# Performance work log

Measured on AMD Instinct MI355X. Metric: run time of the kernel, lower is better.

## Reference

```python
import jax, jax.numpy as jnp
import numpy as np

N_NODES = 100000
N_EDGES = 1600000
F_IN, H1, H2, N_CLS = 512, 180, 120, 40
NEG_SLOPE = 0.01  # F.leaky_relu default


def setup_inputs() -> dict:
    key = jax.random.key(0)
    ks = jax.random.split(key, 8)
    x = jax.random.normal(ks[0], (N_NODES, F_IN), dtype=jnp.float32)
    edge_index = jax.random.randint(ks[1], (2, N_EDGES), 0, N_NODES, dtype=jnp.int64)
    W1 = jax.random.normal(ks[2], (F_IN, H1), dtype=jnp.float32) / np.sqrt(F_IN)
    b1 = jnp.zeros((H1,), dtype=jnp.float32)
    W2 = jax.random.normal(ks[3], (H1, H2), dtype=jnp.float32) / np.sqrt(H1)
    b2 = jnp.zeros((H2,), dtype=jnp.float32)
    W3 = jax.random.normal(ks[4], (H2, N_CLS), dtype=jnp.float32) / np.sqrt(H2)
    b3 = jnp.zeros((N_CLS,), dtype=jnp.float32)
    return {"x": x, "edge_index": edge_index, "W1": W1, "b1": b1,
            "W2": W2, "b2": b2, "W3": W3, "b3": b3}


def _add_self_loops(edge_index, n):
    loop = jnp.arange(n, dtype=edge_index.dtype)
    src = jnp.concatenate([edge_index[0], loop])
    dst = jnp.concatenate([edge_index[1], loop])
    return src, dst


def _gcn_conv(h, src, dst, norm, W, b, n):
    # PyG GCNConv: linear transform first, then normalized scatter-add at dst.
    h = h @ W  # [N, out]
    msg = norm[:, None] * h[src]  # gather at source, per-edge scale
    out = jax.ops.segment_sum(msg, dst, num_segments=n)  # scatter-add at dest
    return out + b


def reference(x, edge_index, W1, b1, W2, b2, W3, b3):
    n = x.shape[0]
    src, dst = _add_self_loops(edge_index, n)
    # symmetric normalization deg^-1/2 * deg^-1/2 on self-loop-augmented graph
    ones = jnp.ones(dst.shape[0], dtype=x.dtype)
    deg = jax.ops.segment_sum(ones, dst, num_segments=n)
    dinv = jnp.where(deg > 0, jax.lax.rsqrt(deg), 0.0)
    norm = dinv[src] * dinv[dst]  # [E+N]

    h = _gcn_conv(x, src, dst, norm, W1, b1, n)
    h = jnp.where(h >= 0, h, NEG_SLOPE * h)
    h = _gcn_conv(h, src, dst, norm, W2, b2, n)
    h = jnp.where(h >= 0, h, NEG_SLOPE * h)
    logits = h @ W3 + b3
    return jax.nn.log_softmax(logits, axis=1)
```

## Files before the change

kernel.cpp:

```cpp
#include <hip/hip_runtime.h>
#include <math.h>

typedef __attribute__((ext_vector_type(8))) short short8;
typedef __attribute__((ext_vector_type(4))) float f32x4;

static constexpr int F_IN = 512;
static constexpr int H1V = 180, H1P = 192;
static constexpr int H2V = 120, H2P = 128;
static constexpr int NC  = 40,  NCP = 64;

__device__ inline unsigned f2bf(float f) {
    unsigned u = __float_as_uint(f);
    return (u + 0x7fffu + ((u >> 16) & 1u)) >> 16;
}
__device__ inline unsigned cvtpk(float lo, float hi) {
    unsigned r;
    asm("v_cvt_pk_bf16_f32 %0, %1, %2" : "=v"(r) : "v"(lo), "v"(hi));
    return r;
}
#define BLO(u) __uint_as_float((u) << 16)
#define BHI(u) __uint_as_float((u) & 0xffff0000u)

__device__ inline void gload_lds16(const void* gsrc, void* ldst) {
    __builtin_amdgcn_global_load_lds(
        (const __attribute__((address_space(1))) void*)gsrc,
        (__attribute__((address_space(3))) void*)ldst, 16, 0, 0);
}

__global__ void k_init(const int* __restrict__ ei, int* __restrict__ flag,
                       const float* __restrict__ W1, const float* __restrict__ W2,
                       const float* __restrict__ W3, const float* __restrict__ b1,
                       const float* __restrict__ b2, const float* __restrict__ b3,
                       unsigned short* __restrict__ W1s, unsigned short* __restrict__ W2s,
                       unsigned short* __restrict__ W3s, float* __restrict__ b1p,
                       float* __restrict__ b2p, float* __restrict__ b3p) {
    if (blockIdx.x < 16) {
        int i = blockIdx.x * 256 + threadIdx.x;
        if (ei[2 * i + 1] != 0) flag[0] = 1;
        return;
    }
    const int n1 = F_IN * H1P;
    const int n2 = n1 + H1P * H2P;
    const int n3 = n2 + H2P * NCP;
    const int n4 = n3 + H1P;
    const int n5 = n4 + H2P;
    const int n6 = n5 + NCP;
    int i = (blockIdx.x - 16) * 256 + threadIdx.x;
    if (i < n1) {
        int k = i / H1P, c = i % H1P;
        float v = (c < H1V) ? W1[k * H1V + c] : 0.0f;
        W1s[(size_t)(k >> 3) * H1P * 8 + c * 8 + (k & 7)] = (unsigned short)f2bf(v);
    } else if (i < n2) {
        int j = i - n1;
        int k = j / H2P, c = j % H2P;
        float v = (k < H1V && c < H2V) ? W2[k * H2V + c] : 0.0f;
        W2s[(size_t)(k >> 3) * H2P * 8 + c * 8 + (k & 7)] = (unsigned short)f2bf(v);
    } else if (i < n3) {
        int j = i - n2;
        int k = j / NCP, c = j % NCP;
        float v = (k < H2V && c < NC) ? W3[k * NC + c] : 0.0f;
        W3s[(size_t)(k >> 3) * NCP * 8 + c * 8 + (k & 7)] = (unsigned short)f2bf(v);
    } else if (i < n4) {
        int c = i - n3;
        b1p[c] = (c < H1V) ? b1[c] : 0.0f;
    } else if (i < n5) {
        int c = i - n4;
        b2p[c] = (c < H2V) ? b2[c] : 0.0f;
    } else if (i < n6) {
        int c = i - n5;
        b3p[c] = (c < NC) ? b3[c] : -1e30f;
    }
}

__global__ __launch_bounds__(256) void k_megaA(const float* __restrict__ X,
                                               const short8* __restrict__ Bs,
                                               signed char* __restrict__ Hq,
                                               float* __restrict__ sc, int M, int gb,
                                               const int* __restrict__ ei, int E,
                                               const int* __restrict__ flag,
                                               int* __restrict__ deg,
                                               int* __restrict__ dst32,
                                               uint2* __restrict__ sr,
                                               int interleave) {
    __shared__ float ldsf[6144];
    int bid;
    bool isGemm;
    if (interleave) {
        int g = blockIdx.x / 3, r = blockIdx.x % 3;
        if (r == 0) { isGemm = true; bid = g; }
        else        { isGemm = false; bid = g * 2 + r - 1; }
    } else {
        isGemm = (int)blockIdx.x < gb;
        bid = isGemm ? blockIdx.x : blockIdx.x - gb;
    }

    if (!isGemm) {
        int e = bid * 256 + threadIdx.x;
        if (e >= E) return;
        bool i64 = (flag[0] == 0);
        int s, d;
        if (i64) { s = ei[2 * e]; d = ei[2 * E + 2 * e]; }
        else     { s = ei[e];     d = ei[E + e]; }
        int r = atomicAdd(&deg[d], 1);
        dst32[e] = d;
        sr[e] = make_uint2((unsigned)s, (unsigned)r);
        return;
    }

    char* lds = (char*)ldsf;
    int t = threadIdx.x;
    int w = t >> 6, l = t & 63;
    int lr = l & 15, kg = l >> 4;
    int row0 = bid * 32;
    int colb = w * 48;

    f32x4 acc[2][3];
#pragma unroll
    for (int m = 0; m < 2; ++m)
#pragma unroll
        for (int nn = 0; nn < 3; ++nn) acc[m][nn] = (f32x4){0.f, 0.f, 0.f, 0.f};

    auto stage = [&](int kb, int buf) {
#pragma unroll
        for (int j = 0; j < 2; ++j) {
            int o = j * 4096 + t * 16;
            int row = o >> 8;
            int col4 = ((o >> 4) & 15) ^ (row & 15);
            int rowg = row0 + row;
            if (rowg >= M) rowg = M - 1;
            gload_lds16(X + (size_t)rowg * F_IN + kb + col4 * 4,
                        lds + buf * 8192 + j * 4096 + w * 1024);
        }
    };

    short8 breg[2][2][3];
    auto loadB = [&](int ts, int pp) {
#pragma unroll
        for (int kk = 0; kk < 2; ++kk)
#pragma unroll
            for (int nn = 0; nn < 3; ++nn)
                breg[pp][kk][nn] =
                    Bs[(size_t)(ts * 8 + kk * 4 + kg) * H1P + colb + nn * 16 + lr];
    };

    auto compute = [&](int cur, int pp) {
#pragma unroll
        for (int kk = 0; kk < 2; ++kk) {
            short8 a[2];
#pragma unroll
            for (int m = 0; m < 2; ++m) {
                int row = m * 16 + lr;
                char* base = lds + cur * 8192 + row * 256;
                int c0 = kk * 8 + kg * 2;
                float4 v0 = *(const float4*)(base + (((c0 + 0) ^ (row & 15)) * 16));
                float4 v1 = *(const float4*)(base + (((c0 + 1) ^ (row & 15)) * 16));
                union { unsigned u[4]; short8 s; } cu;
                cu.u[0] = cvtpk(v0.x, v0.y);
                cu.u[1] = cvtpk(v0.z, v0.w);
                cu.u[2] = cvtpk(v1.x, v1.y);
                cu.u[3] = cvtpk(v1.z, v1.w);
                a[m] = cu.s;
            }
#pragma unroll
            for (int m = 0; m < 2; ++m)
#pragma unroll
                for (int nn = 0; nn < 3; ++nn)
                    acc[m][nn] = __builtin_amdgcn_mfma_f32_16x16x32_bf16(
                        a[m], breg[pp][kk][nn], acc[m][nn], 0, 0, 0);
        }
    };

    stage(0, 0);
    stage(64, 1);
    loadB(0, 0);
    asm volatile("s_waitcnt vmcnt(8)" ::: "memory");
    __builtin_amdgcn_s_barrier();
    __builtin_amdgcn_sched_barrier(0);

#pragma unroll
    for (int ts = 0; ts < 8; ++ts) {
        if (ts < 6) stage((ts + 2) * 64, (ts + 2) % 3);
        if (ts < 7) loadB(ts + 1, (ts + 1) & 1);
        compute(ts % 3, ts & 1);
        if (ts < 7) {
            if (ts < 6) {
                asm volatile("s_waitcnt vmcnt(8)" ::: "memory");
            } else {
                asm volatile("s_waitcnt vmcnt(6)" ::: "memory");
            }
            __builtin_amdgcn_s_barrier();
            __builtin_amdgcn_sched_barrier(0);
        }
    }

    __syncthreads();
    float* rmaxp = (float*)lds;
#pragma unroll
    for (int m = 0; m < 2; ++m) {
#pragma unroll
        for (int j = 0; j < 4; ++j) {
            int rl = m * 16 + kg * 4 + j;
            float lm = 0.f;
#pragma unroll
            for (int nn = 0; nn < 3; ++nn)
                lm = fmaxf(lm, fabsf(acc[m][nn][j]));
#pragma unroll
            for (int d = 1; d < 16; d <<= 1)
                lm = fmaxf(lm, __shfl_xor(lm, d));
            if (lr == 0) rmaxp[rl * 4 + w] = lm;
        }
    }
    __syncthreads();
#pragma unroll
    for (int m = 0; m < 2; ++m) {
#pragma unroll
        for (int j = 0; j < 4; ++j) {
            int rl = m * 16 + kg * 4 + j;
            int grow = row0 + rl;
            if (grow >= M) continue;
            float rm = fmaxf(fmaxf(rmaxp[rl * 4 + 0], rmaxp[rl * 4 + 1]),
                             fmaxf(rmaxp[rl * 4 + 2], rmaxp[rl * 4 + 3]));
            float inv = (rm > 0.f) ? 127.0f / rm : 0.f;
            if (w == 0 && lr == 0) sc[grow] = rm * (1.0f / 127.0f);
#pragma unroll
            for (int nn = 0; nn < 3; ++nn) {
                float v = acc[m][nn][j] * inv;
                v = fminf(fmaxf(rintf(v), -127.f), 127.f);
                Hq[(size_t)grow * H1P + colb + nn * 16 + lr] = (signed char)(int)v;
            }
        }
    }
}

__global__ void k_scan1(const int* __restrict__ deg, int* __restrict__ rp,
                        int* __restrict__ bsum, float* __restrict__ dinv,
                        const float* __restrict__ sc, float* __restrict__ scd,
                        int n) {
    __shared__ int s[256];
    int t = threadIdx.x;
    int base = blockIdx.x * 1024 + t * 4;
    int v0 = (base + 0 < n) ? deg[base + 0] : 0;
    int v1 = (base + 1 < n) ? deg[base + 1] : 0;
    int v2 = (base + 2 < n) ? deg[base + 2] : 0;
    int v3 = (base + 3 < n) ? deg[base + 3] : 0;
    if (base + 0 < n) { float d = rsqrtf((float)(v0 + 1)); dinv[base + 0] = d; scd[base + 0] = d * sc[base + 0]; }
    if (base + 1 < n) { float d = rsqrtf((float)(v1 + 1)); dinv[base + 1] = d; scd[base + 1] = d * sc[base + 1]; }
    if (base + 2 < n) { float d = rsqrtf((float)(v2 + 1)); dinv[base + 2] = d; scd[base + 2] = d * sc[base + 2]; }
    if (base + 3 < n) { float d = rsqrtf((float)(v3 + 1)); dinv[base + 3] = d; scd[base + 3] = d * sc[base + 3]; }
    int sum = v0 + v1 + v2 + v3;
    s[t] = sum;
    __syncthreads();
    for (int off = 1; off < 256; off <<= 1) {
        int x = (t >= off) ? s[t - off] : 0;
        __syncthreads();
        s[t] += x;
        __syncthreads();
    }
    int run = s[t] - sum;
    if (t == 255) bsum[blockIdx.x] = s[255];
    if (base + 0 < n) rp[base + 0] = run; run += v0;
    if (base + 1 < n) rp[base + 1] = run; run += v1;
    if (base + 2 < n) rp[base + 2] = run; run += v2;
    if (base + 3 < n) rp[base + 3] = run;
}

__global__ void k_scan3(const int* __restrict__ bsum, int* __restrict__ rp,
                        int n, int E, int nb) {
    __shared__ int s[128], ov[128];
    int t = threadIdx.x;
    if (t < 128) {
        int v = (t < nb) ? bsum[t] : 0;
        s[t] = v; ov[t] = v;
    }
    __syncthreads();
    for (int off = 1; off < 128; off <<= 1) {
        int x = 0;
        if (t < 128 && t >= off) x = s[t - off];
        __syncthreads();
        if (t < 128) s[t] += x;
        __syncthreads();
    }
    int i = blockIdx.x * 256 + t;
    if (i < n) {
        int b = i >> 10;
        rp[i] += s[b] - ov[b];
    } else if (i == n) {
        rp[n] = E;
    }
}

__global__ __launch_bounds__(256) void k_fill(const int* __restrict__ dst32,
                                              const uint2* __restrict__ sr, int E,
                                              const int* __restrict__ rp,
                                              int* __restrict__ csr,
                                              int bw, int chunk) {
    int bkt = blockIdx.x & 7;
    int lo = bkt * bw, hi = lo + bw;
    int ch = blockIdx.x >> 3;
    int e0 = ch * chunk;
    int e1 = min(E, e0 + chunk);
    for (int e = e0 + (int)threadIdx.x; e < e1; e += 256) {
        int d = dst32[e];
        if (d >= lo && d < hi) {
            uint2 v = sr[e];
            csr[rp[d] + (int)v.y] = (int)v.x;
        }
    }
}

__global__ __launch_bounds__(256) void k_gat1q(const signed char* __restrict__ Hq,
                                               const float* __restrict__ scd,
                                               const float* __restrict__ dinv,
                                               const int* __restrict__ rp,
                                               const int* __restrict__ csr,
                                               const float* __restrict__ bias,
                                               uint2* __restrict__ out, int n) {
    int wv = threadIdx.x >> 6, l = threadIdx.x & 63;
    int i = blockIdx.x * 4 + wv;
    if (i >= n) return;
    bool act = l < 48;
    int c = act ? l : 0;
    const unsigned* Hr = (const unsigned*)(Hq + c * 4);

    float a0, a1, a2, a3;
    {
        unsigned w0 = Hr[(size_t)i * 48];
        float s0 = scd[i];
        a0 = (float)(signed char)(w0) * s0;
        a1 = (float)(signed char)(w0 >> 8) * s0;
        a2 = (float)(signed char)(w0 >> 16) * s0;
        a3 = (float)(signed char)(w0 >> 24) * s0;
    }
    float p0 = 0.f, p1 = 0.f, p2 = 0.f, p3 = 0.f;

    int e0 = rp[i], e1 = rp[i + 1];
    int e = e0;
    for (; e + 7 < e1; e += 8) {
        int s[8];
#pragma unroll
        for (int q = 0; q < 8; ++q) s[q] = csr[e + q];
        float scs[8];
#pragma unroll
        for (int q = 0; q < 8; ++q) scs[q] = scd[s[q]];
        unsigned v[8];
#pragma unroll
        for (int q = 0; q < 8; ++q) v[q] = Hr[(size_t)s[q] * 48];
#pragma unroll
        for (int q = 0; q < 8; q += 2) {
            a0 = fmaf((float)(signed char)(v[q]), scs[q], a0);
            a1 = fmaf((float)(signed char)(v[q] >> 8), scs[q], a1);
            a2 = fmaf((float)(signed char)(v[q] >> 16), scs[q], a2);
            a3 = fmaf((float)(signed char)(v[q] >> 24), scs[q], a3);
            p0 = fmaf((float)(signed char)(v[q + 1]), scs[q + 1], p0);
            p1 = fmaf((float)(signed char)(v[q + 1] >> 8), scs[q + 1], p1);
            p2 = fmaf((float)(signed char)(v[q + 1] >> 16), scs[q + 1], p2);
            p3 = fmaf((float)(signed char)(v[q + 1] >> 24), scs[q + 1], p3);
        }
    }
    for (; e < e1; ++e) {
        int s0 = csr[e];
        float sq = scd[s0];
        unsigned w0 = Hr[(size_t)s0 * 48];
        a0 = fmaf((float)(signed char)(w0), sq, a0);
        a1 = fmaf((float)(signed char)(w0 >> 8), sq, a1);
        a2 = fmaf((float)(signed char)(w0 >> 16), sq, a2);
        a3 = fmaf((float)(signed char)(w0 >> 24), sq, a3);
    }
    a0 += p0; a1 += p1; a2 += p2; a3 += p3;

    float di = dinv[i];
    float4 bb = *(const float4*)(bias + 4 * c);
    float o0 = fmaf(di, a0, bb.x);
    float o1 = fmaf(di, a1, bb.y);
    float o2 = fmaf(di, a2, bb.z);
    float o3 = fmaf(di, a3, bb.w);
    o0 = o0 >= 0.f ? o0 : 0.01f * o0;
    o1 = o1 >= 0.f ? o1 : 0.01f * o1;
    o2 = o2 >= 0.f ? o2 : 0.01f * o2;
    o3 = o3 >= 0.f ? o3 : 0.01f * o3;
    if (act) {
        uint2 r;
        r.x = (f2bf(o1) << 16) | f2bf(o0);
        r.y = (f2bf(o3) << 16) | f2bf(o2);
        out[(size_t)i * 48 + c] = r;
    }
}

__global__ __launch_bounds__(512) void k_gemm2(const unsigned short* __restrict__ A,
                                               const short8* __restrict__ Bs,
                                               const float* __restrict__ dinv,
                                               unsigned short* __restrict__ Hout,
                                               int M) {
    __shared__ unsigned short ldsu[16384];
    char* lds = (char*)ldsu;
    int t = threadIdx.x;
    int w = t >> 6, l = t & 63;
    int lr = l & 15, kg = l >> 4;
    int wr = w >> 2, wc = w & 3;
    int row0 = blockIdx.x * 128;
    int colb = wc * 32;

    f32x4 acc[4][2];
#pragma unroll
    for (int m = 0; m < 4; ++m)
#pragma unroll
        for (int nn = 0; nn < 2; ++nn) acc[m][nn] = (f32x4){0.f, 0.f, 0.f, 0.f};

    auto stage = [&](int kb, int buf) {
#pragma unroll
        for (int j = 0; j < 2; ++j) {
            int o = j * 8192 + t * 16;
            int row = o >> 7;
            int chunk = ((o >> 4) & 7) ^ (row & 7);
            int rowg = row0 + row;
            if (rowg >= M) rowg = M - 1;
            gload_lds16(A + (size_t)rowg * H1P + kb + chunk * 8,
                        lds + buf * 16384 + j * 8192 + w * 1024);
        }
    };

    stage(0, 0);
    __syncthreads();

    for (int ts = 0; ts < 3; ++ts) {
        int cur = ts & 1;
        if (ts < 2) stage((ts + 1) * 64, cur ^ 1);
        short8 b[2][2];
#pragma unroll
        for (int kk = 0; kk < 2; ++kk)
#pragma unroll
            for (int nn = 0; nn < 2; ++nn)
                b[kk][nn] = Bs[(size_t)(ts * 8 + kk * 4 + kg) * H2P + colb + nn * 16 + lr];
        short8 a[2][4];
#pragma unroll
        for (int kk = 0; kk < 2; ++kk)
#pragma unroll
            for (int m = 0; m < 4; ++m) {
                int row = wr * 64 + m * 16 + lr;
                a[kk][m] = *(const short8*)(lds + cur * 16384 + row * 128 +
                                            (((kk * 4 + kg) ^ (row & 7)) * 16));
            }
#pragma unroll
        for (int kk = 0; kk < 2; ++kk)
#pragma unroll
            for (int m = 0; m < 4; ++m)
#pragma unroll
                for (int nn = 0; nn < 2; ++nn)
                    acc[m][nn] = __builtin_amdgcn_mfma_f32_16x16x32_bf16(a[kk][m], b[kk][nn], acc[m][nn], 0, 0, 0);
        __syncthreads();
    }

#pragma unroll
    for (int m = 0; m < 4; ++m) {
        int r4 = row0 + wr * 64 + m * 16 + kg * 4;
#pragma unroll
        for (int j = 0; j < 4; ++j) {
            int grow = r4 + j;
            if (grow < M) {
                float dv = dinv[grow];
#pragma unroll
                for (int nn = 0; nn < 2; ++nn)
                    Hout[(size_t)grow * H2P + colb + nn * 16 + lr] =
                        (unsigned short)f2bf(acc[m][nn][j] * dv);
            }
        }
    }
}

__global__ __launch_bounds__(256) void k_gat2(const uint2* __restrict__ H,
                                              const float* __restrict__ dinv,
                                              const int* __restrict__ rp,
                                              const int* __restrict__ csr,
                                              const float* __restrict__ bias,
                                              uint2* __restrict__ out, int n) {
    int wv = threadIdx.x >> 6, l = threadIdx.x & 63;
    int half = l >> 5, c = l & 31;
    int i = blockIdx.x * 8 + wv * 2 + half;
    if (i >= n) return;
    const uint2* Hr = H + c;

    float a0, a1, a2, a3;
    {
        uint2 v = Hr[(size_t)i * 32];
        a0 = BLO(v.x); a1 = BHI(v.x); a2 = BLO(v.y); a3 = BHI(v.y);
    }
    float p0 = 0.f, p1 = 0.f, p2 = 0.f, p3 = 0.f;

    int e0 = rp[i], e1 = rp[i + 1];
    int e = e0;
    for (; e + 7 < e1; e += 8) {
        int s[8];
#pragma unroll
        for (int q = 0; q < 8; ++q) s[q] = csr[e + q];
        uint2 v[8];
#pragma unroll
        for (int q = 0; q < 8; ++q) v[q] = Hr[(size_t)s[q] * 32];
#pragma unroll
        for (int q = 0; q < 8; q += 2) {
            a0 += BLO(v[q].x); a1 += BHI(v[q].x); a2 += BLO(v[q].y); a3 += BHI(v[q].y);
            p0 += BLO(v[q + 1].x); p1 += BHI(v[q + 1].x); p2 += BLO(v[q + 1].y); p3 += BHI(v[q + 1].y);
        }
    }
    for (; e + 3 < e1; e += 4) {
        int s0 = csr[e], s1 = csr[e + 1], s2 = csr[e + 2], s3 = csr[e + 3];
        uint2 va = Hr[(size_t)s0 * 32];
        uint2 vb = Hr[(size_t)s1 * 32];
        uint2 vc = Hr[(size_t)s2 * 32];
        uint2 vd = Hr[(size_t)s3 * 32];
        a0 += BLO(va.x); a1 += BHI(va.x); a2 += BLO(va.y); a3 += BHI(va.y);
        p0 += BLO(vb.x); p1 += BHI(vb.x); p2 += BLO(vb.y); p3 += BHI(vb.y);
        a0 += BLO(vc.x); a1 += BHI(vc.x); a2 += BLO(vc.y); a3 += BHI(vc.y);
        p0 += BLO(vd.x); p1 += BHI(vd.x); p2 += BLO(vd.y); p3 += BHI(vd.y);
    }
    for (; e < e1; ++e) {
        int s0 = csr[e];
        uint2 va = Hr[(size_t)s0 * 32];
        a0 += BLO(va.x); a1 += BHI(va.x); a2 += BLO(va.y); a3 += BHI(va.y);
    }
    a0 += p0; a1 += p1; a2 += p2; a3 += p3;

    float di = dinv[i];
    float4 bb = *(const float4*)(bias + 4 * c);
    float o0 = fmaf(di, a0, bb.x);
    float o1 = fmaf(di, a1, bb.y);
    float o2 = fmaf(di, a2, bb.z);
    float o3 = fmaf(di, a3, bb.w);
    o0 = o0 >= 0.f ? o0 : 0.01f * o0;
    o1 = o1 >= 0.f ? o1 : 0.01f * o1;
    o2 = o2 >= 0.f ? o2 : 0.01f * o2;
    o3 = o3 >= 0.f ? o3 : 0.01f * o3;
    uint2 r;
    r.x = (f2bf(o1) << 16) | f2bf(o0);
    r.y = (f2bf(o3) << 16) | f2bf(o2);
    out[(size_t)i * 32 + c] = r;
}

__global__ __launch_bounds__(256) void k_out(const unsigned short* __restrict__ H,
                                             const short8* __restrict__ Bs,
                                             const float* __restrict__ b3p,
                                             float* __restrict__ out, int M) {
    int t = threadIdx.x;
    int w = t >> 6, l = t & 63;
    int lr = l & 15, kg = l >> 4;
    int row0 = blockIdx.x * 64 + w * 16;

    f32x4 acc[4];
#pragma unroll
    for (int f = 0; f < 4; ++f) acc[f] = (f32x4){0.f, 0.f, 0.f, 0.f};

    int rowa = row0 + lr;
    if (rowa >= M) rowa = M - 1;
    const unsigned short* arow = H + (size_t)rowa * H2P;

#pragma unroll
    for (int ks = 0; ks < 4; ++ks) {
        short8 a = *(const short8*)(arow + ks * 32 + kg * 8);
#pragma unroll
        for (int f = 0; f < 4; ++f) {
            short8 b = Bs[(size_t)(ks * 4 + kg) * NCP + f * 16 + lr];
            acc[f] = __builtin_amdgcn_mfma_f32_16x16x32_bf16(a, b, acc[f], 0, 0, 0);
        }
    }

    float bl[4];
#pragma unroll
    for (int f = 0; f < 4; ++f) bl[f] = b3p[f * 16 + lr];

#pragma unroll
    for (int j = 0; j < 4; ++j) {
        int grow = row0 + kg * 4 + j;
        float lg[4];
#pragma unroll
        for (int f = 0; f < 4; ++f) lg[f] = acc[f][j] + bl[f];
        float m = fmaxf(fmaxf(lg[0], lg[1]), fmaxf(lg[2], lg[3]));
#pragma unroll
        for (int d = 1; d < 16; d <<= 1) m = fmaxf(m, __shfl_xor(m, d));
        float s = expf(lg[0] - m) + expf(lg[1] - m) + expf(lg[2] - m) + expf(lg[3] - m);
#pragma unroll
        for (int d = 1; d < 16; d <<= 1) s += __shfl_xor(s, d);
        float lse = m + logf(s);
        if (grow < M) {
#pragma unroll
            for (int f = 0; f < 4; ++f) {
                int c = f * 16 + lr;
                if (c < NC) out[(size_t)grow * NC + c] = lg[f] - lse;
            }
        }
    }
}

extern "C" void kernel_launch(void* const* d_in, const int* in_sizes, int n_in,
                              void* d_out, int out_size, void* d_ws, size_t ws_size,
                              hipStream_t stream) {
    const float* x  = (const float*)d_in[0];
    const int*   ei = (const int*)d_in[1];
    const float* W1 = (const float*)d_in[2];
    const float* b1 = (const float*)d_in[3];
    const float* W2 = (const float*)d_in[4];
    const float* b2 = (const float*)d_in[5];
    const float* W3 = (const float*)d_in[6];
    const float* b3 = (const float*)d_in[7];
    float* outp = (float*)d_out;

    int n = in_sizes[0] / F_IN;
    int E = in_sizes[1] / 2;

    char* p = (char*)d_ws;
    auto alloc = [&](size_t bytes) -> char* {
        char* r = p;
        p += (bytes + 511) & ~(size_t)511;
        return r;
    };
    int*            fd     = (int*)alloc((size_t)(n + 1) * 4);
    int*            flag   = fd;
    int*            deg    = fd + 1;
    float*          dinv   = (float*)alloc((size_t)n * 4);
    int*            rp     = (int*)alloc((size_t)(n + 1) * 4);
    int*            bsum   = (int*)alloc(4096);
    int*            dst32  = (int*)alloc((size_t)E * 4);
    uint2*          sr     = (uint2*)alloc((size_t)E * 8);
    int*            csr    = (int*)alloc((size_t)E * 4);
    unsigned short* W1s    = (unsigned short*)alloc((size_t)F_IN * H1P * 2);
    unsigned short* W2s    = (unsigned short*)alloc((size_t)H1P * H2P * 2);
    unsigned short* W3s    = (unsigned short*)alloc((size_t)H2P * NCP * 2);
    float*          b1p    = (float*)alloc(H1P * 4);
    float*          b2p    = (float*)alloc(H2P * 4);
    float*          b3p    = (float*)alloc(NCP * 4);
    signed char*    h1q    = (signed char*)alloc((size_t)n * H1P);
    float*          sc     = (float*)alloc((size_t)n * 4);
    float*          scd    = (float*)alloc((size_t)n * 4);
    unsigned short* h1agg  = (unsigned short*)alloc((size_t)n * H1P * 2);
    unsigned short* h2     = (unsigned short*)alloc((size_t)n * H2P * 2);
    unsigned short* h2agg  = (unsigned short*)alloc((size_t)n * H2P * 2);

    hipMemsetAsync(fd, 0, (size_t)(n + 1) * 4, stream);

    k_init<<<530, 256, 0, stream>>>(ei, flag, W1, W2, W3, b1, b2, b3,
                                    W1s, W2s, W3s, b1p, b2p, b3p);

    int gb = (n + 31) / 32;
    int eb = (E + 255) / 256;
    int interleave = (eb == 2 * gb) ? 1 : 0;
    k_megaA<<<gb + eb, 256, 0, stream>>>(x, (const short8*)W1s, h1q, sc, n, gb,
                                         ei, E, flag, deg, dst32, sr, interleave);

    int nb = (n + 1023) / 1024;
    k_scan1<<<nb, 256, 0, stream>>>(deg, rp, bsum, dinv, sc, scd, n);
    k_scan3<<<(n + 1 + 255) / 256, 256, 0, stream>>>(bsum, rp, n, E, nb);

    int bw = (n + 7) / 8;
    int nch = 256;
    int chunk = (E + nch - 1) / nch;
    k_fill<<<nch * 8, 256, 0, stream>>>(dst32, sr, E, rp, csr, bw, chunk);

    k_gat1q<<<(n + 3) / 4, 256, 0, stream>>>(h1q, scd, dinv, rp, csr, b1p,
                                             (uint2*)h1agg, n);
    k_gemm2<<<(n + 127) / 128, 512, 0, stream>>>(h1agg, (const short8*)W2s, dinv, h2, n);
    k_gat2<<<(n + 7) / 8, 256, 0, stream>>>((const uint2*)h2, dinv, rp, csr, b2p,
                                            (uint2*)h2agg, n);
    k_out<<<(n + 63) / 64, 256, 0, stream>>>(h2agg, (const short8*)W3s, b3p, outp, n);
}
```

Before: 316.7 us.

## Load GEMM A operand directly into registers instead of staging through LDS

The first-layer GEMM used to stage X tiles into a triple-buffered LDS ring with global_load_lds and barriers. It now loads each lane's fp32 A fragment straight from global memory into registers, converts it to bf16, and prefetches the next k-step one iteration ahead. This drops the LDS traffic and the per-step block barriers and shrinks shared memory to 128 floats, which may raise occupancy. In exchange, each wave fetches A in a less coalesced pattern, and the full vmcnt(0) wait every step may expose global load latency.

New measurement: 380.6 us. 1.2x slower.

```diff
diff --git a/kernel.cpp b/kernel.cpp
--- a/kernel.cpp
+++ b/kernel.cpp
@@ -82,7 +82,7 @@
                                                int* __restrict__ dst32,
                                                uint2* __restrict__ sr,
                                                int interleave) {
-    __shared__ float ldsf[6144];
+    __shared__ float rmaxp[128];
     int bid;
     bool isGemm;
     if (interleave) {
@@ -107,7 +107,6 @@
         return;
     }
 
-    char* lds = (char*)ldsf;
     int t = threadIdx.x;
     int w = t >> 6, l = t & 63;
     int lr = l & 15, kg = l >> 4;
@@ -120,16 +119,22 @@
 #pragma unroll
         for (int nn = 0; nn < 3; ++nn) acc[m][nn] = (f32x4){0.f, 0.f, 0.f, 0.f};
 
-    auto stage = [&](int kb, int buf) {
-#pragma unroll
-        for (int j = 0; j < 2; ++j) {
-            int o = j * 4096 + t * 16;
-            int row = o >> 8;
-            int col4 = ((o >> 4) & 15) ^ (row & 15);
-            int rowg = row0 + row;
-            if (rowg >= M) rowg = M - 1;
-            gload_lds16(X + (size_t)rowg * F_IN + kb + col4 * 4,
-                        lds + buf * 8192 + j * 4096 + w * 1024);
+    int r0 = row0 + lr;      if (r0 >= M) r0 = M - 1;
+    int r1 = row0 + 16 + lr; if (r1 >= M) r1 = M - 1;
+    const float* __restrict__ pA0 = X + (size_t)r0 * F_IN + kg * 8;
+    const float* __restrict__ pA1 = X + (size_t)r1 * F_IN + kg * 8;
+
+    float4 araw[8];
+    auto loadA = [&](int ts) {
+        int kb = ts * 64;
+#pragma unroll
+        for (int kk = 0; kk < 2; ++kk) {
+            const float* a0 = pA0 + kb + kk * 32;
+            const float* a1 = pA1 + kb + kk * 32;
+            araw[(0 * 2 + kk) * 2 + 0] = *(const float4*)(a0);
+            araw[(0 * 2 + kk) * 2 + 1] = *(const float4*)(a0 + 4);
+            araw[(1 * 2 + kk) * 2 + 0] = *(const float4*)(a1);
+            araw[(1 * 2 + kk) * 2 + 1] = *(const float4*)(a1 + 4);
         }
     };
 
@@ -143,58 +148,40 @@
                     Bs[(size_t)(ts * 8 + kk * 4 + kg) * H1P + colb + nn * 16 + lr];
     };
 
-    auto compute = [&](int cur, int pp) {
-#pragma unroll
-        for (int kk = 0; kk < 2; ++kk) {
-            short8 a[2];
-#pragma unroll
-            for (int m = 0; m < 2; ++m) {
-                int row = m * 16 + lr;
-                char* base = lds + cur * 8192 + row * 256;
-                int c0 = kk * 8 + kg * 2;
-                float4 v0 = *(const float4*)(base + (((c0 + 0) ^ (row & 15)) * 16));
-                float4 v1 = *(const float4*)(base + (((c0 + 1) ^ (row & 15)) * 16));
-                union { unsigned u[4]; short8 s; } cu;
-                cu.u[0] = cvtpk(v0.x, v0.y);
-                cu.u[1] = cvtpk(v0.z, v0.w);
-                cu.u[2] = cvtpk(v1.x, v1.y);
-                cu.u[3] = cvtpk(v1.z, v1.w);
-                a[m] = cu.s;
-            }
+    loadA(0);
+    loadB(0, 0);
+    asm volatile("s_waitcnt vmcnt(0)" ::: "memory");
+
+#pragma unroll
+    for (int ts = 0; ts < 8; ++ts) {
+        short8 abf[4];
+#pragma unroll
+        for (int idx = 0; idx < 4; ++idx) {
+            float4 v0 = araw[idx * 2 + 0];
+            float4 v1 = araw[idx * 2 + 1];
+            union { unsigned u[4]; short8 s; } cu;
+            cu.u[0] = cvtpk(v0.x, v0.y);
+            cu.u[1] = cvtpk(v0.z, v0.w);
+            cu.u[2] = cvtpk(v1.x, v1.y);
+            cu.u[3] = cvtpk(v1.z, v1.w);
+            abf[idx] = cu.s;
+        }
+        if (ts < 7) {
+            loadA(ts + 1);
+            loadB(ts + 1, (ts + 1) & 1);
+        }
+        int pp = ts & 1;
+#pragma unroll
+        for (int kk = 0; kk < 2; ++kk)
 #pragma unroll
             for (int m = 0; m < 2; ++m)
 #pragma unroll
                 for (int nn = 0; nn < 3; ++nn)
                     acc[m][nn] = __builtin_amdgcn_mfma_f32_16x16x32_bf16(
-                        a[m], breg[pp][kk][nn], acc[m][nn], 0, 0, 0);
-        }
-    };
-
-    stage(0, 0);
-    stage(64, 1);
-    loadB(0, 0);
-    asm volatile("s_waitcnt vmcnt(8)" ::: "memory");
-    __builtin_amdgcn_s_barrier();
-    __builtin_amdgcn_sched_barrier(0);
-
-#pragma unroll
-    for (int ts = 0; ts < 8; ++ts) {
-        if (ts < 6) stage((ts + 2) * 64, (ts + 2) % 3);
-        if (ts < 7) loadB(ts + 1, (ts + 1) & 1);
-        compute(ts % 3, ts & 1);
-        if (ts < 7) {
-            if (ts < 6) {
-                asm volatile("s_waitcnt vmcnt(8)" ::: "memory");
-            } else {
-                asm volatile("s_waitcnt vmcnt(6)" ::: "memory");
-            }
-            __builtin_amdgcn_s_barrier();
-            __builtin_amdgcn_sched_barrier(0);
-        }
-    }
-
-    __syncthreads();
-    float* rmaxp = (float*)lds;
+                        abf[m * 2 + kk], breg[pp][kk][nn], acc[m][nn], 0, 0, 0);
+        if (ts < 7) asm volatile("s_waitcnt vmcnt(0)" ::: "memory");
+    }
+
 #pragma unroll
     for (int m = 0; m < 2; ++m) {
 #pragma unroll
```
